# Optimization experiments

Measured on AMD Instinct MI355X. Metric: run time of the kernel, lower is better.

Reference implementation:

```python
import jax, jax.numpy as jnp
import numpy as np


def rotate_half(x):
    x1, x2 = jnp.split(x, 2, axis=-1)
    return jnp.concatenate((-x2, x1), axis=-1)


def setup_inputs() -> dict:
    key = jax.random.key(0)
    ks = jax.random.split(key, 8)
    B, S, H, C = 4, 2048, 2048, 512
    QK = H + C
    NH = 16
    dqk = QK // NH  # 160
    return {
        "hidden_states": jax.random.normal(ks[0], (B, S, H), jnp.float32),
        "cond_states": jax.random.normal(ks[1], (B, S, C), jnp.float32),
        "cos": jax.random.uniform(ks[2], (S, dqk), jnp.float32),
        "sin": jax.random.uniform(ks[3], (S, dqk), jnp.float32),
        "Wq": jax.random.normal(ks[4], (QK, QK), jnp.float32) * 0.02,
        "Wk": jax.random.normal(ks[5], (QK, QK), jnp.float32) * 0.02,
        "Wv": jax.random.normal(ks[6], (H, H), jnp.float32) * 0.02,
        "Wo": jax.random.normal(ks[7], (H, H), jnp.float32) * 0.02,
    }


def reference(hidden_states, cond_states, cos, sin, Wq, Wk, Wv, Wo):
    B, S, H = hidden_states.shape
    NH = 16
    qk_in = jnp.concatenate([hidden_states, cond_states], axis=-1)  # [B,S,QK]
    q = (qk_in @ Wq.T).reshape(B, S, NH, -1)  # [B,S,NH,dqk]
    k = (qk_in @ Wk.T).reshape(B, S, NH, -1)
    v = (hidden_states @ Wv.T).reshape(B, S, NH, -1)  # [B,S,NH,dv]
    # RoPE in fp32; cos/sin broadcast over batch and heads: (S,1,dqk)
    cos_b = cos[:, None, :].astype(jnp.float32)
    sin_b = sin[:, None, :].astype(jnp.float32)
    qf, kf = q.astype(jnp.float32), k.astype(jnp.float32)
    q = (qf * cos_b + rotate_half(qf) * sin_b).astype(q.dtype)
    k = (kf * cos_b + rotate_half(kf) * sin_b).astype(k.dtype)
    dqk = q.shape[-1]
    scale = 1.0 / jnp.sqrt(jnp.asarray(dqk, q.dtype))
    scores = jnp.einsum("bqhd,bkhd->bhqk", q, k) * scale  # [B,NH,S,S]
    probs = jax.nn.softmax(scores, axis=-1)
    attn = jnp.einsum("bhqk,bkhd->bqhd", probs, v)  # [B,S,NH,dv]
    attn = attn.reshape(B, S, -1)
    return attn @ Wo.T
```

## Files before the change

kernel.cpp:

```cpp
#include <hip/hip_runtime.h>
#include <cstdint>
#include <cstddef>

typedef __attribute__((ext_vector_type(8))) short bf16x8;
typedef __attribute__((ext_vector_type(4))) short bf16x4;
typedef __attribute__((ext_vector_type(4))) float f32x4;

#define MFMA_BF16 __builtin_amdgcn_mfma_f32_16x16x32_bf16

constexpr int B_   = 4;
constexpr int S_   = 2048;
constexpr int H_   = 2048;
constexpr int C_   = 512;
constexpr int QKD  = 2560;
constexpr int NH   = 16;
constexpr int DQK  = 160;
constexpr int DV   = 128;
constexpr int MTOT = B_ * S_;

static __device__ __forceinline__ short f2bf(float f) {
  unsigned u = __builtin_bit_cast(unsigned, f);
  u += 0x7FFFu + ((u >> 16) & 1u);
  return (short)(u >> 16);
}
static __device__ __forceinline__ float bf2f(short h) {
  unsigned u = ((unsigned)(unsigned short)h) << 16;
  return __builtin_bit_cast(float, u);
}
static __device__ __forceinline__ void gload_lds16(const void* g, void* l) {
  __builtin_amdgcn_global_load_lds((const __attribute__((address_space(1))) unsigned*)g,
                                   (__attribute__((address_space(3))) unsigned*)l, 16, 0, 0);
}

__global__ __launch_bounds__(256) void k_build_qkin(const float* __restrict__ hidden,
                                                    const float* __restrict__ cond,
                                                    short* __restrict__ qk) {
  int i = blockIdx.x * 256 + threadIdx.x;
  int row = i / (QKD / 4);
  int c4  = i - row * (QKD / 4);
  f32x4 v;
  if (c4 < H_ / 4) v = *((const f32x4*)hidden + (size_t)row * (H_ / 4) + c4);
  else             v = *((const f32x4*)cond   + (size_t)row * (C_ / 4) + (c4 - H_ / 4));
  bf16x4 o;
  o[0] = f2bf(v[0]); o[1] = f2bf(v[1]); o[2] = f2bf(v[2]); o[3] = f2bf(v[3]);
  *(bf16x4*)(qk + (size_t)row * QKD + c4 * 4) = o;
}

__global__ __launch_bounds__(256) void k_cvt_bf16(const float* __restrict__ in,
                                                  short* __restrict__ out) {
  size_t i = (size_t)blockIdx.x * 256 + threadIdx.x;
  f32x4 v = *((const f32x4*)in + i);
  bf16x4 o;
  o[0] = f2bf(v[0]); o[1] = f2bf(v[1]); o[2] = f2bf(v[2]); o[3] = f2bf(v[3]);
  *(bf16x4*)(out + i * 4) = o;
}

template<int MODE>
__global__ __launch_bounds__(256) void k_gemm_bt(const short* __restrict__ A,
                                                 const short* __restrict__ W,
                                                 void* __restrict__ Cp,
                                                 int N, int K, int lda) {
  __shared__ short lA[128 * 32];
  __shared__ short lB[128 * 32];
  const int tid = threadIdx.x;
  const int lane = tid & 63, wid = tid >> 6;
  const int m0 = blockIdx.y * 128, n0 = blockIdx.x * 128;
  const int wr = wid >> 1, wc = wid & 1;
  const int l15 = lane & 15, l4 = lane >> 4;
  f32x4 acc[4][4] = {};

  const int srow = lane >> 2;
  const int scol = (lane & 3) * 8;
  const short* Abase = A + (size_t)m0 * lda;
  const short* Wbase = W + (size_t)n0 * K;
  const int nkt = K >> 5;

  for (int kt = 0; kt < nkt; ++kt) {
    const int k0 = kt << 5;
#pragma unroll
    for (int i = 0; i < 2; ++i) {
      int c = wid * 2 + i;
      gload_lds16(Abase + (size_t)(c * 16 + srow) * lda + k0 + scol, &lA[c * 512]);
      gload_lds16(Wbase + (size_t)(c * 16 + srow) * K   + k0 + scol, &lB[c * 512]);
    }
    __syncthreads();
    bf16x8 af[4], bv[4];
#pragma unroll
    for (int x = 0; x < 4; ++x) {
      af[x] = *(const bf16x8*)&lA[(wr * 64 + x * 16 + l15) * 32 + l4 * 8];
      bv[x] = *(const bf16x8*)&lB[(wc * 64 + x * 16 + l15) * 32 + l4 * 8];
    }
#pragma unroll
    for (int mi = 0; mi < 4; ++mi)
#pragma unroll
      for (int nj = 0; nj < 4; ++nj)
        acc[mi][nj] = MFMA_BF16(af[mi], bv[nj], acc[mi][nj], 0, 0, 0);
    __syncthreads();
  }

#pragma unroll
  for (int mi = 0; mi < 4; ++mi) {
#pragma unroll
    for (int nj = 0; nj < 4; ++nj) {
      int crow = m0 + wr * 64 + mi * 16 + l4 * 4;
      int ccol = n0 + wc * 64 + nj * 16 + l15;
      if constexpr (MODE == 0) {
        int b = crow >> 11;
        int s = crow - (b << 11);
        int h = ccol / DQK;
        int d = ccol - h * DQK;
        short* dst = (short*)Cp + ((size_t)(b * NH + h) * S_) * DQK + d;
#pragma unroll
        for (int r = 0; r < 4; ++r)
          dst[(size_t)(s + r) * DQK] = f2bf(acc[mi][nj][r]);
      } else if constexpr (MODE == 1) {
        int b = crow >> 11;
        int s = crow - (b << 11);
        int h = ccol >> 7;
        int d = ccol & 127;
        short* dst = (short*)Cp + ((size_t)(b * NH + h) * DV + d) * S_ + s;
        bf16x4 o;
        o[0] = f2bf(acc[mi][nj][0]); o[1] = f2bf(acc[mi][nj][1]);
        o[2] = f2bf(acc[mi][nj][2]); o[3] = f2bf(acc[mi][nj][3]);
        *(bf16x4*)dst = o;
      } else {
        float* dst = (float*)Cp + (size_t)crow * N + ccol;
#pragma unroll
        for (int r = 0; r < 4; ++r) dst[(size_t)r * N] = acc[mi][nj][r];
      }
    }
  }
}

__global__ __launch_bounds__(256) void k_rope(short* __restrict__ x,
                                              const float* __restrict__ cs,
                                              const float* __restrict__ sn) {
  int i = blockIdx.x * 256 + threadIdx.x;
  int c4   = i % 20;
  int rest = i / 20;
  int s  = rest & (S_ - 1);
  int bh = rest >> 11;
  size_t base = ((size_t)bh * S_ + s) * DQK;
  int d = c4 * 4;
  bf16x4 x1 = *(bf16x4*)(x + base + d);
  bf16x4 x2 = *(bf16x4*)(x + base + d + 80);
  f32x4 c1 = *(const f32x4*)(cs + (size_t)s * DQK + d);
  f32x4 s1 = *(const f32x4*)(sn + (size_t)s * DQK + d);
  f32x4 c2 = *(const f32x4*)(cs + (size_t)s * DQK + d + 80);
  f32x4 s2 = *(const f32x4*)(sn + (size_t)s * DQK + d + 80);
  bf16x4 o1, o2;
#pragma unroll
  for (int j = 0; j < 4; ++j) {
    float a = bf2f(x1[j]), b = bf2f(x2[j]);
    o1[j] = f2bf(a * c1[j] - b * s1[j]);
    o2[j] = f2bf(b * c2[j] + a * s2[j]);
  }
  *(bf16x4*)(x + base + d)      = o1;
  *(bf16x4*)(x + base + d + 80) = o2;
}

__global__ __launch_bounds__(256) void k_attn(const short* __restrict__ q,
                                              const short* __restrict__ k,
                                              const short* __restrict__ vt,
                                              short* __restrict__ attn) {
  __shared__ short lK[64 * 160];
  __shared__ short lV[128 * 64];
  __shared__ short lP[4 * 32 * 64];
  const int tid = threadIdx.x, lane = tid & 63, wid = tid >> 6;
  const int bh = blockIdx.y, b = bh >> 4, h = bh & 15;
  const int q0 = blockIdx.x * 128;
  const short* Q  = q  + (size_t)bh * S_ * DQK;
  const char*  Kb = (const char*)(k + (size_t)bh * S_ * DQK);
  const char*  Vb = (const char*)(vt + (size_t)bh * DV * S_);
  const int l15 = lane & 15, l4 = lane >> 4;

  bf16x8 qf[2][5];
#pragma unroll
  for (int mi = 0; mi < 2; ++mi)
#pragma unroll
    for (int ks = 0; ks < 5; ++ks)
      qf[mi][ks] = *(const bf16x8*)(Q + (size_t)(q0 + wid * 32 + mi * 16 + l15) * DQK + ks * 32 + l4 * 8);

  f32x4 acc[2][8] = {};
  float mrow[2][4], lrow[2][4];
#pragma unroll
  for (int mi = 0; mi < 2; ++mi)
#pragma unroll
    for (int r = 0; r < 4; ++r) { mrow[mi][r] = -1e30f; lrow[mi][r] = 0.f; }
  const float csc = 0.07905694150420949f * 1.44269504089f;

  for (int kv0 = 0; kv0 < S_; kv0 += 64) {
#pragma unroll
    for (int i = 0; i < 5; ++i) {
      int c = wid * 5 + i;
      int off = c * 1024 + lane * 16;
      int row = off / 320;
      int colB = off - row * 320;
      gload_lds16(Kb + (size_t)(kv0 + row) * 320 + colB, &lK[c * 512]);
    }
#pragma unroll
    for (int i = 0; i < 4; ++i) {
      int c = wid * 4 + i;
      int row = c * 8 + (lane >> 3);
      int cb  = (lane & 7) ^ (lane >> 3);
      gload_lds16(Vb + (size_t)row * (S_ * 2) + kv0 * 2 + cb * 16, &lV[c * 512]);
    }
    __syncthreads();

    f32x4 sc[2][4] = {};
#pragma unroll
    for (int kj = 0; kj < 4; ++kj) {
#pragma unroll
      for (int ks = 0; ks < 5; ++ks) {
        bf16x8 kf = *(const bf16x8*)&lK[(kj * 16 + l15) * 160 + ks * 32 + l4 * 8];
        sc[0][kj] = MFMA_BF16(qf[0][ks], kf, sc[0][kj], 0, 0, 0);
        sc[1][kj] = MFMA_BF16(qf[1][ks], kf, sc[1][kj], 0, 0, 0);
      }
    }

#pragma unroll
    for (int mi = 0; mi < 2; ++mi) {
      float pm[4];
#pragma unroll
      for (int r = 0; r < 4; ++r)
        pm[r] = fmaxf(fmaxf(sc[mi][0][r], sc[mi][1][r]), fmaxf(sc[mi][2][r], sc[mi][3][r]));
#pragma unroll
      for (int m = 1; m < 16; m <<= 1)
#pragma unroll
        for (int r = 0; r < 4; ++r) pm[r] = fmaxf(pm[r], __shfl_xor(pm[r], m, 64));
#pragma unroll
      for (int r = 0; r < 4; ++r) {
        float mn = fmaxf(mrow[mi][r], pm[r] * csc);
        float al = exp2f(mrow[mi][r] - mn);
        mrow[mi][r] = mn;
        lrow[mi][r] *= al;
#pragma unroll
        for (int nf = 0; nf < 8; ++nf) acc[mi][nf][r] *= al;
        int prow = mi * 16 + l4 * 4 + r;
        int pxor = (prow & 7) << 4;
#pragma unroll
        for (int kj = 0; kj < 4; ++kj) {
          float p = exp2f(sc[mi][kj][r] * csc - mn);
          lrow[mi][r] += p;
          *(short*)((char*)lP + wid * 4096 + prow * 128 + ((kj * 32 + l15 * 2) ^ pxor)) = f2bf(p);
        }
      }
    }

#pragma unroll
    for (int kc = 0; kc < 2; ++kc) {
      bf16x8 pa[2];
#pragma unroll
      for (int mi = 0; mi < 2; ++mi) {
        int row = mi * 16 + l15;
        pa[mi] = *(const bf16x8*)((const char*)lP + wid * 4096 + row * 128 +
                                  ((kc * 64 + l4 * 16) ^ ((row & 7) << 4)));
      }
#pragma unroll
      for (int nf = 0; nf < 8; ++nf) {
        int row = nf * 16 + l15;
        bf16x8 vf = *(const bf16x8*)((const char*)lV + row * 128 +
                                     ((kc * 64 + l4 * 16) ^ ((row & 7) << 4)));
        acc[0][nf] = MFMA_BF16(pa[0], vf, acc[0][nf], 0, 0, 0);
        acc[1][nf] = MFMA_BF16(pa[1], vf, acc[1][nf], 0, 0, 0);
      }
    }
    __syncthreads();
  }

#pragma unroll
  for (int mi = 0; mi < 2; ++mi)
#pragma unroll
    for (int r = 0; r < 4; ++r) {
      float s = lrow[mi][r];
#pragma unroll
      for (int m = 1; m < 16; m <<= 1) s += __shfl_xor(s, m, 64);
      lrow[mi][r] = 1.0f / s;
    }
#pragma unroll
  for (int mi = 0; mi < 2; ++mi)
#pragma unroll
    for (int nf = 0; nf < 8; ++nf) {
      size_t col = (size_t)h * DV + nf * 16 + l15;
#pragma unroll
      for (int r = 0; r < 4; ++r) {
        int mg = q0 + wid * 32 + mi * 16 + l4 * 4 + r;
        attn[(size_t)(b * S_ + mg) * H_ + col] = f2bf(acc[mi][nf][r] * lrow[mi][r]);
      }
    }
}

extern "C" void kernel_launch(void* const* d_in, const int* in_sizes, int n_in,
                              void* d_out, int out_size, void* d_ws, size_t ws_size,
                              hipStream_t stream) {
  const float* hidden = (const float*)d_in[0];
  const float* cond   = (const float*)d_in[1];
  const float* cosp   = (const float*)d_in[2];
  const float* sinp   = (const float*)d_in[3];
  const float* Wq     = (const float*)d_in[4];
  const float* Wk     = (const float*)d_in[5];
  const float* Wv     = (const float*)d_in[6];
  const float* Wo     = (const float*)d_in[7];

  constexpr size_t SZ_QKIN = (size_t)MTOT * QKD * 2;
  constexpr size_t SZ_VT   = (size_t)MTOT * H_ * 2;
  constexpr size_t SZ_WBF  = (size_t)QKD * QKD * 2;
  constexpr size_t WS_NEED = SZ_QKIN * 3 + SZ_VT + SZ_WBF;
  if (ws_size < WS_NEED) return;

  char* ws = (char*)d_ws;
  short* qk_in = (short*)(ws);
  short* qbuf  = (short*)(ws + SZ_QKIN);
  short* kbuf  = (short*)(ws + 2 * SZ_QKIN);
  short* vtbuf = (short*)(ws + 3 * SZ_QKIN);
  short* w_bf  = (short*)(ws + 3 * SZ_QKIN + SZ_VT);
  short* attn  = qk_in;
  float* outp  = (float*)d_out;

  k_build_qkin<<<(MTOT * QKD / 4) / 256, 256, 0, stream>>>(hidden, cond, qk_in);

  dim3 gq(QKD / 128, MTOT / 128);
  dim3 gv(H_ / 128, MTOT / 128);

  k_cvt_bf16<<<(QKD * QKD / 4) / 256, 256, 0, stream>>>(Wq, w_bf);
  k_gemm_bt<0><<<gq, 256, 0, stream>>>(qk_in, w_bf, qbuf, QKD, QKD, QKD);

  k_cvt_bf16<<<(QKD * QKD / 4) / 256, 256, 0, stream>>>(Wk, w_bf);
  k_gemm_bt<0><<<gq, 256, 0, stream>>>(qk_in, w_bf, kbuf, QKD, QKD, QKD);

  k_cvt_bf16<<<(H_ * H_ / 4) / 256, 256, 0, stream>>>(Wv, w_bf);
  k_gemm_bt<1><<<gv, 256, 0, stream>>>(qk_in, w_bf, vtbuf, H_, H_, QKD);

  k_rope<<<(B_ * NH * S_ * 20) / 256, 256, 0, stream>>>(qbuf, cosp, sinp);
  k_rope<<<(B_ * NH * S_ * 20) / 256, 256, 0, stream>>>(kbuf, cosp, sinp);

  dim3 ga(S_ / 128, B_ * NH);
  k_attn<<<ga, 256, 0, stream>>>(qbuf, kbuf, vtbuf, attn);

  k_cvt_bf16<<<(H_ * H_ / 4) / 256, 256, 0, stream>>>(Wo, w_bf);
  k_gemm_bt<2><<<gv, 256, 0, stream>>>(attn, w_bf, outp, H_, H_, H_);
}
```

Before: 1.038 ms.

## Transpose QK MFMA, lazily rescale softmax, swizzle K LDS, remap workgroups across XCDs

```diff
diff --git a/kernel.cpp b/kernel.cpp
--- a/kernel.cpp
+++ b/kernel.cpp
@@ -26,6 +26,11 @@
 static __device__ __forceinline__ float bf2f(short h) {
   unsigned u = ((unsigned)(unsigned short)h) << 16;
   return __builtin_bit_cast(float, u);
+}
+static __device__ __forceinline__ unsigned cvt_pk_bf16(float a, float b) {
+  unsigned r;
+  asm("v_cvt_pk_bf16_f32 %0, %1, %2" : "=v"(r) : "v"(a), "v"(b));
+  return r;
 }
 static __device__ __forceinline__ void gload_lds16(const void* g, void* l) {
   __builtin_amdgcn_global_load_lds((const __attribute__((address_space(1))) unsigned*)g,
@@ -64,7 +69,12 @@
   __shared__ short lB[128 * 32];
   const int tid = threadIdx.x;
   const int lane = tid & 63, wid = tid >> 6;
-  const int m0 = blockIdx.y * 128, n0 = blockIdx.x * 128;
+  const int gx = gridDim.x, gy = gridDim.y;
+  const int nwg = gx * gy, cpx = nwg >> 3;
+  const int wg  = blockIdx.y * gx + blockIdx.x;
+  const int wg2 = (wg & 7) * cpx + (wg >> 3);
+  const int xb  = wg2 / gy, yb = wg2 - xb * gy;
+  const int m0 = yb * 128, n0 = xb * 128;
   const int wr = wid >> 1, wc = wid & 1;
   const int l15 = lane & 15, l4 = lane >> 4;
   f32x4 acc[4][4] = {};
@@ -167,8 +177,10 @@
   __shared__ short lV[128 * 64];
   __shared__ short lP[4 * 32 * 64];
   const int tid = threadIdx.x, lane = tid & 63, wid = tid >> 6;
-  const int bh = blockIdx.y, b = bh >> 4, h = bh & 15;
-  const int q0 = blockIdx.x * 128;
+  const int wg  = blockIdx.y * gridDim.x + blockIdx.x;
+  const int wg2 = (wg & 7) * 128 + (wg >> 3);
+  const int bh  = wg2 >> 4, b = bh >> 4, h = bh & 15;
+  const int q0  = (wg2 & 15) * 128;
   const short* Q  = q  + (size_t)bh * S_ * DQK;
   const char*  Kb = (const char*)(k + (size_t)bh * S_ * DQK);
   const char*  Vb = (const char*)(vt + (size_t)bh * DV * S_);
@@ -182,22 +194,27 @@
       qf[mi][ks] = *(const bf16x8*)(Q + (size_t)(q0 + wid * 32 + mi * 16 + l15) * DQK + ks * 32 + l4 * 8);
 
   f32x4 acc[2][8] = {};
-  float mrow[2][4], lrow[2][4];
-#pragma unroll
-  for (int mi = 0; mi < 2; ++mi)
-#pragma unroll
-    for (int r = 0; r < 4; ++r) { mrow[mi][r] = -1e30f; lrow[mi][r] = 0.f; }
+  float mrow[2], lrow[2];
+#pragma unroll
+  for (int mi = 0; mi < 2; ++mi) { mrow[mi] = -1e30f; lrow[mi] = 0.f; }
   const float csc = 0.07905694150420949f * 1.44269504089f;
 
+  int koff[5], kcolS[5];
+#pragma unroll
+  for (int i = 0; i < 5; ++i) {
+    int c = wid * 5 + i;
+    int off = c * 1024 + lane * 16;
+    int row = off / 320;
+    int colB = off - row * 320;
+    int g = colB >> 4;
+    int colS = (g < 16) ? (colB ^ ((row & 7) << 4)) : (colB ^ ((row & 3) << 4));
+    koff[i] = row;  kcolS[i] = colS;
+  }
+
   for (int kv0 = 0; kv0 < S_; kv0 += 64) {
 #pragma unroll
-    for (int i = 0; i < 5; ++i) {
-      int c = wid * 5 + i;
-      int off = c * 1024 + lane * 16;
-      int row = off / 320;
-      int colB = off - row * 320;
-      gload_lds16(Kb + (size_t)(kv0 + row) * 320 + colB, &lK[c * 512]);
-    }
+    for (int i = 0; i < 5; ++i)
+      gload_lds16(Kb + (size_t)(kv0 + koff[i]) * 320 + kcolS[i], &lK[(wid * 5 + i) * 512]);
 #pragma unroll
     for (int i = 0; i < 4; ++i) {
       int c = wid * 4 + i;
@@ -207,43 +224,62 @@
     }
     __syncthreads();
 
-    f32x4 sc[2][4] = {};
+    f32x4 sc[4][2] = {};
 #pragma unroll
     for (int kj = 0; kj < 4; ++kj) {
+      int row = kj * 16 + l15;
+      int x7 = (row & 7) << 4, x3 = (row & 3) << 4;
 #pragma unroll
       for (int ks = 0; ks < 5; ++ks) {
-        bf16x8 kf = *(const bf16x8*)&lK[(kj * 16 + l15) * 160 + ks * 32 + l4 * 8];
-        sc[0][kj] = MFMA_BF16(qf[0][ks], kf, sc[0][kj], 0, 0, 0);
-        sc[1][kj] = MFMA_BF16(qf[1][ks], kf, sc[1][kj], 0, 0, 0);
-      }
-    }
-
+        int colB = (ks < 4) ? ((ks * 64 + l4 * 16) ^ x7) : ((256 + l4 * 16) ^ x3);
+        bf16x8 kf = *(const bf16x8*)((const char*)lK + row * 320 + colB);
+        sc[kj][0] = MFMA_BF16(kf, qf[0][ks], sc[kj][0], 0, 0, 0);
+        sc[kj][1] = MFMA_BF16(kf, qf[1][ks], sc[kj][1], 0, 0, 0);
+      }
+    }
+
+    float pms[2];
 #pragma unroll
     for (int mi = 0; mi < 2; ++mi) {
-      float pm[4];
-#pragma unroll
-      for (int r = 0; r < 4; ++r)
-        pm[r] = fmaxf(fmaxf(sc[mi][0][r], sc[mi][1][r]), fmaxf(sc[mi][2][r], sc[mi][3][r]));
-#pragma unroll
-      for (int m = 1; m < 16; m <<= 1)
-#pragma unroll
-        for (int r = 0; r < 4; ++r) pm[r] = fmaxf(pm[r], __shfl_xor(pm[r], m, 64));
-#pragma unroll
-      for (int r = 0; r < 4; ++r) {
-        float mn = fmaxf(mrow[mi][r], pm[r] * csc);
-        float al = exp2f(mrow[mi][r] - mn);
-        mrow[mi][r] = mn;
-        lrow[mi][r] *= al;
-#pragma unroll
-        for (int nf = 0; nf < 8; ++nf) acc[mi][nf][r] *= al;
-        int prow = mi * 16 + l4 * 4 + r;
-        int pxor = (prow & 7) << 4;
-#pragma unroll
-        for (int kj = 0; kj < 4; ++kj) {
-          float p = exp2f(sc[mi][kj][r] * csc - mn);
-          lrow[mi][r] += p;
-          *(short*)((char*)lP + wid * 4096 + prow * 128 + ((kj * 32 + l15 * 2) ^ pxor)) = f2bf(p);
+      float mv = sc[0][mi][0];
+#pragma unroll
+      for (int kj = 0; kj < 4; ++kj)
+#pragma unroll
+        for (int r = 0; r < 4; ++r) mv = fmaxf(mv, sc[kj][mi][r]);
+      mv = fmaxf(mv, __shfl_xor(mv, 16, 64));
+      mv = fmaxf(mv, __shfl_xor(mv, 32, 64));
+      pms[mi] = mv * csc;
+    }
+    if (__any((pms[0] > mrow[0] + 8.0f) || (pms[1] > mrow[1] + 8.0f))) {
+#pragma unroll
+      for (int mi = 0; mi < 2; ++mi) {
+        float mn = fmaxf(mrow[mi], pms[mi]);
+        float al = exp2f(mrow[mi] - mn);
+        mrow[mi] = mn; lrow[mi] *= al;
+#pragma unroll
+        for (int r = 0; r < 4; ++r) {
+          float alr = __shfl(al, (lane & 48) | (l4 * 4 + r), 64);
+#pragma unroll
+          for (int nf = 0; nf < 8; ++nf) acc[mi][nf][r] *= alr;
         }
+      }
+    }
+#pragma unroll
+    for (int mi = 0; mi < 2; ++mi) {
+      int qrow = mi * 16 + l15;
+      char* lpb = (char*)lP + wid * 4096 + qrow * 128;
+      int xq = (qrow & 7) << 4;
+#pragma unroll
+      for (int kj = 0; kj < 4; ++kj) {
+        float p0 = exp2f(sc[kj][mi][0] * csc - mrow[mi]);
+        float p1 = exp2f(sc[kj][mi][1] * csc - mrow[mi]);
+        float p2 = exp2f(sc[kj][mi][2] * csc - mrow[mi]);
+        float p3 = exp2f(sc[kj][mi][3] * csc - mrow[mi]);
+        lrow[mi] += (p0 + p1) + (p2 + p3);
+        uint2 w;
+        w.x = cvt_pk_bf16(p0, p1);
+        w.y = cvt_pk_bf16(p2, p3);
+        *(uint2*)(lpb + ((kj * 32 + l4 * 8) ^ xq)) = w;
       }
     }
 
@@ -268,15 +304,17 @@
     __syncthreads();
   }
 
-#pragma unroll
-  for (int mi = 0; mi < 2; ++mi)
-#pragma unroll
-    for (int r = 0; r < 4; ++r) {
-      float s = lrow[mi][r];
-#pragma unroll
-      for (int m = 1; m < 16; m <<= 1) s += __shfl_xor(s, m, 64);
-      lrow[mi][r] = 1.0f / s;
-    }
+  float invr[2][4];
+#pragma unroll
+  for (int mi = 0; mi < 2; ++mi) {
+    float s = lrow[mi];
+    s += __shfl_xor(s, 16, 64);
+    s += __shfl_xor(s, 32, 64);
+    float inv = 1.0f / s;
+#pragma unroll
+    for (int r = 0; r < 4; ++r)
+      invr[mi][r] = __shfl(inv, (lane & 48) | (l4 * 4 + r), 64);
+  }
 #pragma unroll
   for (int mi = 0; mi < 2; ++mi)
 #pragma unroll
@@ -285,7 +323,7 @@
 #pragma unroll
       for (int r = 0; r < 4; ++r) {
         int mg = q0 + wid * 32 + mi * 16 + l4 * 4 + r;
-        attn[(size_t)(b * S_ + mg) * H_ + col] = f2bf(acc[mi][nf][r] * lrow[mi][r]);
+        attn[(size_t)(b * S_ + mg) * H_ + col] = f2bf(acc[mi][nf][r] * invr[mi][r]);
       }
     }
 }
```

Result: faster. 967.6 us (-6.8%).
